# Optimization experiments

Measured on AMD Instinct MI355X. Metric: run time of the kernel, lower is better.

## Reference

```python
import jax, jax.numpy as jnp
import numpy as np

N_NODES = 100000
N_EDGES = 3200000
EMBED_DIM = 64
BATCH = 16384


def setup_inputs() -> dict:
    key = jax.random.key(0)
    k1, k2, k3, k4 = jax.random.split(key, 4)
    gcn_weight = jax.random.normal(k1, (N_NODES, EMBED_DIM), dtype=jnp.float32) * 0.1
    gcn_bias = jnp.zeros((EMBED_DIM,), dtype=jnp.float32)
    linear_weight = jax.random.normal(k2, (N_NODES, 1), dtype=jnp.float32) * 0.1
    linear_bias = jnp.zeros((1,), dtype=jnp.float32)
    edge_index = jax.random.randint(k3, (2, N_EDGES), 0, N_NODES, dtype=jnp.int64)
    interaction_pairs = jax.random.randint(k4, (BATCH, 2), 0, N_NODES, dtype=jnp.int64)
    return {
        "gcn_weight": gcn_weight,
        "gcn_bias": gcn_bias,
        "linear_weight": linear_weight,
        "linear_bias": linear_bias,
        "edge_index": edge_index,
        "interaction_pairs": interaction_pairs,
    }


def _gcn_conv_identity_features(gcn_weight, gcn_bias, edge_index):
    # Features X = I, so X @ W = W. GCNConv output = D^{-1/2}(A+I)D^{-1/2} W + b.
    src, dst = edge_index[0], edge_index[1]
    ones = jnp.ones((src.shape[0],), dtype=gcn_weight.dtype)
    # degree (with self loop) computed on destination nodes, as in PyG gcn_norm
    deg = jax.ops.segment_sum(ones, dst, num_segments=N_NODES) + 1.0
    dinv = jax.lax.rsqrt(deg)  # [N]
    norm = dinv[src] * dinv[dst]  # [E]
    msg = gcn_weight[src] * norm[:, None]  # [E, D] -- dominant memory traffic
    agg = jax.ops.segment_sum(msg, dst, num_segments=N_NODES)  # [N, D]
    # self-loop term: norm_ii = 1/deg[i]
    out = agg + gcn_weight * (dinv * dinv)[:, None] + gcn_bias
    return out


def reference(gcn_weight, gcn_bias, linear_weight, linear_bias, edge_index, interaction_pairs):
    node_emb = _gcn_conv_identity_features(gcn_weight, gcn_bias, edge_index)  # [N, D]
    e = node_emb[interaction_pairs]  # [B, 2, D] gather
    # FM pairwise interaction: 0.5 * sum_d ((sum_f e)^2 - sum_f e^2)
    sum_sq = jnp.square(jnp.sum(e, axis=1))  # [B, D]
    sq_sum = jnp.sum(jnp.square(e), axis=1)  # [B, D]
    fm = 0.5 * jnp.sum(sum_sq - sq_sum, axis=1, keepdims=True)  # [B, 1]
    # FeaturesLinear: sum of per-node scalar embeddings + bias
    lin = jnp.sum(linear_weight[interaction_pairs], axis=1) + linear_bias  # [B, 1]
    return jnp.squeeze(lin + fm, axis=1)  # [B]
```

## Files before the change

kernel.cpp:

```cpp
#include <hip/hip_runtime.h>

#define N_NODES 100000
#define N_EDGES 3200000
#define BATCH 16384
#define MAX_SLOTS 32768

#define NW 12500
#define SLICES 256
#define EPS2 12500
#define I4PS2 3125

#define NBUCK 256
#define BSH 7

#define OFF_SLOT      0
#define OFF_DINV      400064
#define OFF_NODELIST  800064
#define OFF_BTOT      931136
#define OFF_BPART     932160
#define OFF_SLOTSTART 1194304
#define OFF_PARTIALS  1325440
#define OFF_WH        14125440
#define OFF_BINS      26925440
#define OFF_BINS2     31725440
#define OFF_EMB       36525440

__device__ __forceinline__ unsigned bfr(float f) {
    unsigned u = __float_as_uint(f);
    return (u + 0x7FFFu + ((u >> 16) & 1u)) >> 16;
}
__device__ __forceinline__ float bfx(unsigned h) {
    return __uint_as_float(h << 16);
}

__global__ void k_flags(const int* __restrict__ pairs, unsigned* __restrict__ slot,
                        int* __restrict__ nodelist) {
    int i = blockIdx.x * blockDim.x + threadIdx.x;
    if (i < 2 * BATCH) {
        int n = pairs[i];
        nodelist[i] = n;
        slot[n] = (unsigned)(i + 1);
    }
}

__device__ __forceinline__ int cert(int d, const unsigned* __restrict__ slot,
                                    const int* __restrict__ nodelist) {
    unsigned r = slot[d];
    unsigned idx = r - 1u;
    if (idx < (unsigned)MAX_SLOTS && nodelist[idx] == d) return (int)idx;
    return -1;
}

__global__ void k_hist(const int* __restrict__ dst, const unsigned* __restrict__ slot,
                       const int* __restrict__ nodelist,
                       unsigned* __restrict__ partials, int* __restrict__ bpart) {
    __shared__ unsigned h[NW];
    __shared__ int lc[NBUCK];
    int g = blockIdx.x;
    for (int i = threadIdx.x; i < NW; i += 512) h[i] = 0;
    if (threadIdx.x < NBUCK) lc[threadIdx.x] = 0;
    __syncthreads();
    const int4* d4 = (const int4*)(dst + g * EPS2);
    for (int i = threadIdx.x; i < I4PS2; i += 512) {
        int4 v = d4[i];
        atomicAdd(&h[v.x >> 3], 1u << ((v.x & 7) << 2));
        atomicAdd(&h[v.y >> 3], 1u << ((v.y & 7) << 2));
        atomicAdd(&h[v.z >> 3], 1u << ((v.z & 7) << 2));
        atomicAdd(&h[v.w >> 3], 1u << ((v.w & 7) << 2));
        int t;
        t = cert(v.x, slot, nodelist); if (t >= 0) atomicAdd(&lc[t >> BSH], 1);
        t = cert(v.y, slot, nodelist); if (t >= 0) atomicAdd(&lc[t >> BSH], 1);
        t = cert(v.z, slot, nodelist); if (t >= 0) atomicAdd(&lc[t >> BSH], 1);
        t = cert(v.w, slot, nodelist); if (t >= 0) atomicAdd(&lc[t >> BSH], 1);
    }
    __syncthreads();
    unsigned* outp = partials + (unsigned)g * NW;
    for (int i = threadIdx.x; i < NW; i += 512) outp[i] = h[i];
    if (threadIdx.x < NBUCK) bpart[threadIdx.x * SLICES + g] = lc[threadIdx.x];
}

__global__ void k_mid(const unsigned* __restrict__ partials, const float4* __restrict__ w4,
                      float* __restrict__ dinv, uint4* __restrict__ wh4,
                      int* __restrict__ bpart, int* __restrict__ btot) {
    if (blockIdx.x >= 391) {
        __shared__ int t[SLICES];
        int b = blockIdx.x - 391, g = threadIdx.x;
        int v = bpart[b * SLICES + g];
        t[g] = v;
        __syncthreads();
        for (int off = 1; off < SLICES; off <<= 1) {
            int x = (g >= off) ? t[g - off] : 0;
            __syncthreads();
            t[g] += x;
            __syncthreads();
        }
        bpart[b * SLICES + g] = t[g] - v;
        if (g == SLICES - 1) btot[b] = t[g];
        return;
    }
    __shared__ unsigned pA[256], pB[256], pC[256], pD[256];
    __shared__ float sdinv[256];
    int blk = blockIdx.x;
    int wi = threadIdx.x & 31, sg = threadIdx.x >> 5;
    int w = blk * 32 + wi;
    unsigned A = 0, B = 0, C = 0, D = 0;
    if (w < NW) {
        const unsigned* q = partials + w;
#pragma unroll
        for (int ch = 0; ch < 2; ++ch) {
            unsigned x = 0, y = 0;
#pragma unroll
            for (int k = 0; k < 16; ++k) {
                unsigned v = q[(unsigned)(sg * 32 + ch * 16 + k) * NW];
                x += v & 0x0F0F0F0Fu;
                y += (v >> 4) & 0x0F0F0F0Fu;
            }
            A += x & 0x00FF00FFu;
            B += (x >> 8) & 0x00FF00FFu;
            C += y & 0x00FF00FFu;
            D += (y >> 8) & 0x00FF00FFu;
        }
    }
    pA[threadIdx.x] = A; pB[threadIdx.x] = B; pC[threadIdx.x] = C; pD[threadIdx.x] = D;
    __syncthreads();
    if (threadIdx.x < 32 && w < NW) {
        unsigned sA = 0, sB = 0, sC = 0, sD = 0;
#pragma unroll
        for (int k = 0; k < 8; ++k) {
            sA += pA[k * 32 + wi]; sB += pB[k * 32 + wi];
            sC += pC[k * 32 + wi]; sD += pD[k * 32 + wi];
        }
        float4 d0, d1;
        d0.x = rsqrtf((float)(sA & 0xFFFFu) + 1.0f);
        d0.y = rsqrtf((float)(sC & 0xFFFFu) + 1.0f);
        d0.z = rsqrtf((float)(sB & 0xFFFFu) + 1.0f);
        d0.w = rsqrtf((float)(sD & 0xFFFFu) + 1.0f);
        d1.x = rsqrtf((float)(sA >> 16) + 1.0f);
        d1.y = rsqrtf((float)(sC >> 16) + 1.0f);
        d1.z = rsqrtf((float)(sB >> 16) + 1.0f);
        d1.w = rsqrtf((float)(sD >> 16) + 1.0f);
        ((float4*)dinv)[w * 2] = d0;
        ((float4*)dinv)[w * 2 + 1] = d1;
        int lb = wi * 8;
        sdinv[lb + 0] = d0.x; sdinv[lb + 1] = d0.y; sdinv[lb + 2] = d0.z; sdinv[lb + 3] = d0.w;
        sdinv[lb + 4] = d1.x; sdinv[lb + 5] = d1.y; sdinv[lb + 6] = d1.z; sdinv[lb + 7] = d1.w;
    }
    __syncthreads();
#pragma unroll
    for (int it = 0; it < 8; ++it) {
        int k = blk * 2048 + it * 256 + threadIdx.x;
        if (k < N_NODES * 8) {
            float4 va = w4[k * 2];
            float4 vb = w4[k * 2 + 1];
            float d = sdinv[(k >> 3) - blk * 256];
            uint4 o;
            o.x = bfr(va.x * d) | (bfr(va.y * d) << 16);
            o.y = bfr(va.z * d) | (bfr(va.w * d) << 16);
            o.z = bfr(vb.x * d) | (bfr(vb.y * d) << 16);
            o.w = bfr(vb.z * d) | (bfr(vb.w * d) << 16);
            wh4[k] = o;
        }
    }
}

__global__ void k_bscatter(const int* __restrict__ src, const int* __restrict__ dst,
                           const unsigned* __restrict__ slot, const int* __restrict__ nodelist,
                           const int* __restrict__ bpart, const int* __restrict__ btot,
                           int* __restrict__ bins) {
    __shared__ int tb[NBUCK], vv[NBUCK], cur[NBUCK];
    int g = blockIdx.x;
    int t = threadIdx.x;
    if (t < NBUCK) { int v = btot[t]; vv[t] = v; tb[t] = v; }
    __syncthreads();
    for (int off = 1; off < NBUCK; off <<= 1) {
        int x = (t < NBUCK && t >= off) ? tb[t - off] : 0;
        __syncthreads();
        if (t < NBUCK) tb[t] += x;
        __syncthreads();
    }
    if (t < NBUCK) cur[t] = tb[t] - vv[t] + bpart[t * SLICES + g];
    __syncthreads();
    const int4* d4 = (const int4*)(dst + g * EPS2);
    const int4* s4 = (const int4*)(src + g * EPS2);
    for (int i = t; i < I4PS2; i += 512) {
        int4 d = d4[i];
        int4 s = s4[i];
        int sl;
        sl = cert(d.x, slot, nodelist);
        if (sl >= 0) { int pos = atomicAdd(&cur[sl >> BSH], 1); bins[pos] = ((sl & 127) << 17) | s.x; }
        sl = cert(d.y, slot, nodelist);
        if (sl >= 0) { int pos = atomicAdd(&cur[sl >> BSH], 1); bins[pos] = ((sl & 127) << 17) | s.y; }
        sl = cert(d.z, slot, nodelist);
        if (sl >= 0) { int pos = atomicAdd(&cur[sl >> BSH], 1); bins[pos] = ((sl & 127) << 17) | s.z; }
        sl = cert(d.w, slot, nodelist);
        if (sl >= 0) { int pos = atomicAdd(&cur[sl >> BSH], 1); bins[pos] = ((sl & 127) << 17) | s.w; }
    }
}

__global__ void k_bsort(const int* __restrict__ btot, const int* __restrict__ bins,
                        int* __restrict__ slotstart, int* __restrict__ bins2) {
    __shared__ int tb[NBUCK], vv[NBUCK];
    __shared__ int lc[128], st[128];
    int b = blockIdx.x;
    int tid = threadIdx.x;
    { int v = btot[tid]; vv[tid] = v; tb[tid] = v; }
    __syncthreads();
    for (int off = 1; off < NBUCK; off <<= 1) {
        int x = (tid >= off) ? tb[tid - off] : 0;
        __syncthreads();
        tb[tid] += x;
        __syncthreads();
    }
    int beg = tb[b] - vv[b];
    int end = beg + vv[b];
    if (tid < 128) lc[tid] = 0;
    __syncthreads();
    for (int j = beg + tid; j < end; j += 256)
        atomicAdd(&lc[(bins[j] >> 17) & 127], 1);
    __syncthreads();
    if (tid < 128) st[tid] = lc[tid];
    __syncthreads();
    for (int off = 1; off < 128; off <<= 1) {
        int v = (tid < 128 && tid >= off) ? st[tid - off] : 0;
        __syncthreads();
        if (tid < 128) st[tid] += v;
        __syncthreads();
    }
    if (tid < 128) {
        int s0 = beg + st[tid] - lc[tid];
        slotstart[(b << 7) + tid] = s0;
        lc[tid] = s0;
    }
    if (b == NBUCK - 1 && tid == 0) slotstart[MAX_SLOTS] = tb[NBUCK - 1];
    __syncthreads();
    for (int j = beg + tid; j < end; j += 256) {
        int e = bins[j];
        int pos = atomicAdd(&lc[(e >> 17) & 127], 1);
        bins2[pos] = e & 0x1FFFF;
    }
}

__global__ void k_gather(const int* __restrict__ nodelist, const int* __restrict__ slotstart,
                         const int* __restrict__ bins2, const uint4* __restrict__ wh4,
                         const float* __restrict__ dinv, const float4* __restrict__ bias4,
                         uint4* __restrict__ emb4) {
    int s = (blockIdx.x * blockDim.x + threadIdx.x) >> 6;
    int lane = threadIdx.x & 63;
    int rg = lane >> 3, dp = lane & 7;
    int beg = slotstart[s], end = slotstart[s + 1];
    float a0 = 0.f, a1 = 0.f, a2 = 0.f, a3 = 0.f, a4 = 0.f, a5 = 0.f, a6 = 0.f, a7 = 0.f;
    int j = beg;
    for (; j + 16 <= end; j += 16) {
        int e0 = bins2[j + rg];
        int e1 = bins2[j + 8 + rg];
        uint4 oa = wh4[(e0 << 3) + dp];
        uint4 ob = wh4[(e1 << 3) + dp];
        a0 += bfx(oa.x) + bfx(ob.x);
        a1 += bfx(oa.x >> 16) + bfx(ob.x >> 16);
        a2 += bfx(oa.y) + bfx(ob.y);
        a3 += bfx(oa.y >> 16) + bfx(ob.y >> 16);
        a4 += bfx(oa.z) + bfx(ob.z);
        a5 += bfx(oa.z >> 16) + bfx(ob.z >> 16);
        a6 += bfx(oa.w) + bfx(ob.w);
        a7 += bfx(oa.w >> 16) + bfx(ob.w >> 16);
    }
    for (; j < end; j += 8) {
        if (rg < end - j) {
            int e0 = bins2[j + rg];
            uint4 oa = wh4[(e0 << 3) + dp];
            a0 += bfx(oa.x); a1 += bfx(oa.x >> 16);
            a2 += bfx(oa.y); a3 += bfx(oa.y >> 16);
            a4 += bfx(oa.z); a5 += bfx(oa.z >> 16);
            a6 += bfx(oa.w); a7 += bfx(oa.w >> 16);
        }
    }
#pragma unroll
    for (int m = 8; m <= 32; m <<= 1) {
        a0 += __shfl_xor(a0, m, 64); a1 += __shfl_xor(a1, m, 64);
        a2 += __shfl_xor(a2, m, 64); a3 += __shfl_xor(a3, m, 64);
        a4 += __shfl_xor(a4, m, 64); a5 += __shfl_xor(a5, m, 64);
        a6 += __shfl_xor(a6, m, 64); a7 += __shfl_xor(a7, m, 64);
    }
    if (rg == 0) {
        int n = nodelist[s];
        float dn = dinv[n];
        uint4 u = wh4[(n << 3) + dp];
        float4 b0 = bias4[dp * 2], b1 = bias4[dp * 2 + 1];
        float r0 = (a0 + bfx(u.x)) * dn + b0.x;
        float r1 = (a1 + bfx(u.x >> 16)) * dn + b0.y;
        float r2 = (a2 + bfx(u.y)) * dn + b0.z;
        float r3 = (a3 + bfx(u.y >> 16)) * dn + b0.w;
        float r4 = (a4 + bfx(u.z)) * dn + b1.x;
        float r5 = (a5 + bfx(u.z >> 16)) * dn + b1.y;
        float r6 = (a6 + bfx(u.w)) * dn + b1.z;
        float r7 = (a7 + bfx(u.w >> 16)) * dn + b1.w;
        uint4 o;
        o.x = bfr(r0) | (bfr(r1) << 16);
        o.y = bfr(r2) | (bfr(r3) << 16);
        o.z = bfr(r4) | (bfr(r5) << 16);
        o.w = bfr(r6) | (bfr(r7) << 16);
        emb4[(s << 3) + dp] = o;
    }
}

__global__ void k_final(const int* __restrict__ pairs, const unsigned* __restrict__ slot,
                        const uint2* __restrict__ emb2, const float* __restrict__ lw,
                        const float* __restrict__ lb, float* __restrict__ out) {
    int p = (blockIdx.x * blockDim.x + threadIdx.x) >> 4;
    int li = threadIdx.x & 15;
    if (p >= BATCH) return;
    int a = pairs[p * 2], b = pairs[p * 2 + 1];
    int sa = (int)slot[a] - 1;
    int sb = (int)slot[b] - 1;
    uint2 ua = emb2[(sa << 4) + li];
    uint2 ub = emb2[(sb << 4) + li];
    float prod = bfx(ua.x) * bfx(ub.x) + bfx(ua.x >> 16) * bfx(ub.x >> 16)
               + bfx(ua.y) * bfx(ub.y) + bfx(ua.y >> 16) * bfx(ub.y >> 16);
#pragma unroll
    for (int m = 1; m <= 8; m <<= 1) prod += __shfl_xor(prod, m, 64);
    if (li == 0) out[p] = lw[a] + lw[b] + lb[0] + prod;
}

extern "C" void kernel_launch(void* const* d_in, const int* in_sizes, int n_in,
                              void* d_out, int out_size, void* d_ws, size_t ws_size,
                              hipStream_t stream) {
    const float* gcn_weight    = (const float*)d_in[0];
    const float* gcn_bias      = (const float*)d_in[1];
    const float* linear_weight = (const float*)d_in[2];
    const float* linear_bias   = (const float*)d_in[3];
    const int*   edge_index    = (const int*)d_in[4];
    const int*   pairs         = (const int*)d_in[5];
    float* out = (float*)d_out;

    char* ws = (char*)d_ws;
    unsigned* slot      = (unsigned*)(ws + OFF_SLOT);
    float*    dinv      = (float*)   (ws + OFF_DINV);
    int*      nodelist  = (int*)     (ws + OFF_NODELIST);
    int*      btot      = (int*)     (ws + OFF_BTOT);
    int*      bpart     = (int*)     (ws + OFF_BPART);
    int*      slotstart = (int*)     (ws + OFF_SLOTSTART);
    unsigned* partials  = (unsigned*)(ws + OFF_PARTIALS);
    uint4*    wh4       = (uint4*)   (ws + OFF_WH);
    int*      bins      = (int*)     (ws + OFF_BINS);
    int*      bins2     = (int*)     (ws + OFF_BINS2);
    uint4*    emb4      = (uint4*)   (ws + OFF_EMB);
    uint2*    emb2      = (uint2*)   (ws + OFF_EMB);

    const int* src_arr = edge_index;
    const int* dst_arr = edge_index + N_EDGES;

    k_flags<<<128, 256, 0, stream>>>(pairs, slot, nodelist);
    k_hist<<<SLICES, 512, 0, stream>>>(dst_arr, slot, nodelist, partials, bpart);
    k_mid<<<391 + 256, 256, 0, stream>>>(partials, (const float4*)gcn_weight, dinv, wh4,
                                         bpart, btot);
    k_bscatter<<<SLICES, 512, 0, stream>>>(src_arr, dst_arr, slot, nodelist, bpart, btot, bins);
    k_bsort<<<NBUCK, 256, 0, stream>>>(btot, bins, slotstart, bins2);
    k_gather<<<MAX_SLOTS / 4, 256, 0, stream>>>(nodelist, slotstart, bins2, wh4,
                                                dinv, (const float4*)gcn_bias, emb4);
    k_final<<<1024, 256, 0, stream>>>(pairs, slot, emb2, linear_weight, linear_bias, out);
}
```

Measured before the change: 185.1 us.

## Replace two-pass bucket sort with fixed-capacity per-slot bins filled in histogram kernel

Drops the bucket count/scan/scatter/sort pipeline (k_bscatter, k_bsort and the scan blocks in k_mid). Edges into batch nodes are now appended straight into fixed 128-entry per-slot bins using global atomic counters, inside the degree-histogram kernel, which now runs 1024-thread blocks. This removes a second pass over the edge list and two kernel launches. The gather now reads the per-slot counts and accumulates in double precision. The fixed capacity silently drops neighbors beyond 128 per node, and double accumulation raises register use and ALU cost.

```diff
diff --git a/kernel.cpp b/kernel.cpp
--- a/kernel.cpp
+++ b/kernel.cpp
@@ -10,20 +10,16 @@
 #define EPS2 12500
 #define I4PS2 3125
 
-#define NBUCK 256
-#define BSH 7
+#define CAP 128
 
 #define OFF_SLOT      0
 #define OFF_DINV      400064
 #define OFF_NODELIST  800064
-#define OFF_BTOT      931136
-#define OFF_BPART     932160
-#define OFF_SLOTSTART 1194304
-#define OFF_PARTIALS  1325440
-#define OFF_WH        14125440
-#define OFF_BINS      26925440
-#define OFF_BINS2     31725440
-#define OFF_EMB       36525440
+#define OFF_SCOUNT    931136
+#define OFF_PARTIALS  1062208
+#define OFF_WH        13862208
+#define OFF_BINS2     26662208
+#define OFF_EMB       43439424
 
 __device__ __forceinline__ unsigned bfr(float f) {
     unsigned u = __float_as_uint(f);
@@ -34,12 +30,13 @@
 }
 
 __global__ void k_flags(const int* __restrict__ pairs, unsigned* __restrict__ slot,
-                        int* __restrict__ nodelist) {
+                        int* __restrict__ nodelist, int* __restrict__ scount) {
     int i = blockIdx.x * blockDim.x + threadIdx.x;
     if (i < 2 * BATCH) {
         int n = pairs[i];
         nodelist[i] = n;
         slot[n] = (unsigned)(i + 1);
+        scount[i] = 0;
     }
 }
 
@@ -51,53 +48,40 @@
     return -1;
 }
 
-__global__ void k_hist(const int* __restrict__ dst, const unsigned* __restrict__ slot,
-                       const int* __restrict__ nodelist,
-                       unsigned* __restrict__ partials, int* __restrict__ bpart) {
+__global__ void k_fused(const int* __restrict__ src, const int* __restrict__ dst,
+                        const unsigned* __restrict__ slot, const int* __restrict__ nodelist,
+                        unsigned* __restrict__ partials,
+                        int* __restrict__ scount, int* __restrict__ bins2) {
     __shared__ unsigned h[NW];
-    __shared__ int lc[NBUCK];
     int g = blockIdx.x;
-    for (int i = threadIdx.x; i < NW; i += 512) h[i] = 0;
-    if (threadIdx.x < NBUCK) lc[threadIdx.x] = 0;
+    for (int i = threadIdx.x; i < NW; i += 1024) h[i] = 0;
     __syncthreads();
     const int4* d4 = (const int4*)(dst + g * EPS2);
-    for (int i = threadIdx.x; i < I4PS2; i += 512) {
+    const int4* s4 = (const int4*)(src + g * EPS2);
+    for (int i = threadIdx.x; i < I4PS2; i += 1024) {
         int4 v = d4[i];
+        int4 s = s4[i];
         atomicAdd(&h[v.x >> 3], 1u << ((v.x & 7) << 2));
         atomicAdd(&h[v.y >> 3], 1u << ((v.y & 7) << 2));
         atomicAdd(&h[v.z >> 3], 1u << ((v.z & 7) << 2));
         atomicAdd(&h[v.w >> 3], 1u << ((v.w & 7) << 2));
         int t;
-        t = cert(v.x, slot, nodelist); if (t >= 0) atomicAdd(&lc[t >> BSH], 1);
-        t = cert(v.y, slot, nodelist); if (t >= 0) atomicAdd(&lc[t >> BSH], 1);
-        t = cert(v.z, slot, nodelist); if (t >= 0) atomicAdd(&lc[t >> BSH], 1);
-        t = cert(v.w, slot, nodelist); if (t >= 0) atomicAdd(&lc[t >> BSH], 1);
+        t = cert(v.x, slot, nodelist);
+        if (t >= 0) { int p = atomicAdd(&scount[t], 1); if (p < CAP) bins2[(t << 7) + p] = s.x; }
+        t = cert(v.y, slot, nodelist);
+        if (t >= 0) { int p = atomicAdd(&scount[t], 1); if (p < CAP) bins2[(t << 7) + p] = s.y; }
+        t = cert(v.z, slot, nodelist);
+        if (t >= 0) { int p = atomicAdd(&scount[t], 1); if (p < CAP) bins2[(t << 7) + p] = s.z; }
+        t = cert(v.w, slot, nodelist);
+        if (t >= 0) { int p = atomicAdd(&scount[t], 1); if (p < CAP) bins2[(t << 7) + p] = s.w; }
     }
     __syncthreads();
     unsigned* outp = partials + (unsigned)g * NW;
-    for (int i = threadIdx.x; i < NW; i += 512) outp[i] = h[i];
-    if (threadIdx.x < NBUCK) bpart[threadIdx.x * SLICES + g] = lc[threadIdx.x];
+    for (int i = threadIdx.x; i < NW; i += 1024) outp[i] = h[i];
 }
 
 __global__ void k_mid(const unsigned* __restrict__ partials, const float4* __restrict__ w4,
-                      float* __restrict__ dinv, uint4* __restrict__ wh4,
-                      int* __restrict__ bpart, int* __restrict__ btot) {
-    if (blockIdx.x >= 391) {
-        __shared__ int t[SLICES];
-        int b = blockIdx.x - 391, g = threadIdx.x;
-        int v = bpart[b * SLICES + g];
-        t[g] = v;
-        __syncthreads();
-        for (int off = 1; off < SLICES; off <<= 1) {
-            int x = (g >= off) ? t[g - off] : 0;
-            __syncthreads();
-            t[g] += x;
-            __syncthreads();
-        }
-        bpart[b * SLICES + g] = t[g] - v;
-        if (g == SLICES - 1) btot[b] = t[g];
-        return;
-    }
+                      float* __restrict__ dinv, uint4* __restrict__ wh4) {
     __shared__ unsigned pA[256], pB[256], pC[256], pD[256];
     __shared__ float sdinv[256];
     int blk = blockIdx.x;
@@ -163,115 +147,39 @@
     }
 }
 
-__global__ void k_bscatter(const int* __restrict__ src, const int* __restrict__ dst,
-                           const unsigned* __restrict__ slot, const int* __restrict__ nodelist,
-                           const int* __restrict__ bpart, const int* __restrict__ btot,
-                           int* __restrict__ bins) {
-    __shared__ int tb[NBUCK], vv[NBUCK], cur[NBUCK];
-    int g = blockIdx.x;
-    int t = threadIdx.x;
-    if (t < NBUCK) { int v = btot[t]; vv[t] = v; tb[t] = v; }
-    __syncthreads();
-    for (int off = 1; off < NBUCK; off <<= 1) {
-        int x = (t < NBUCK && t >= off) ? tb[t - off] : 0;
-        __syncthreads();
-        if (t < NBUCK) tb[t] += x;
-        __syncthreads();
-    }
-    if (t < NBUCK) cur[t] = tb[t] - vv[t] + bpart[t * SLICES + g];
-    __syncthreads();
-    const int4* d4 = (const int4*)(dst + g * EPS2);
-    const int4* s4 = (const int4*)(src + g * EPS2);
-    for (int i = t; i < I4PS2; i += 512) {
-        int4 d = d4[i];
-        int4 s = s4[i];
-        int sl;
-        sl = cert(d.x, slot, nodelist);
-        if (sl >= 0) { int pos = atomicAdd(&cur[sl >> BSH], 1); bins[pos] = ((sl & 127) << 17) | s.x; }
-        sl = cert(d.y, slot, nodelist);
-        if (sl >= 0) { int pos = atomicAdd(&cur[sl >> BSH], 1); bins[pos] = ((sl & 127) << 17) | s.y; }
-        sl = cert(d.z, slot, nodelist);
-        if (sl >= 0) { int pos = atomicAdd(&cur[sl >> BSH], 1); bins[pos] = ((sl & 127) << 17) | s.z; }
-        sl = cert(d.w, slot, nodelist);
-        if (sl >= 0) { int pos = atomicAdd(&cur[sl >> BSH], 1); bins[pos] = ((sl & 127) << 17) | s.w; }
-    }
-}
-
-__global__ void k_bsort(const int* __restrict__ btot, const int* __restrict__ bins,
-                        int* __restrict__ slotstart, int* __restrict__ bins2) {
-    __shared__ int tb[NBUCK], vv[NBUCK];
-    __shared__ int lc[128], st[128];
-    int b = blockIdx.x;
-    int tid = threadIdx.x;
-    { int v = btot[tid]; vv[tid] = v; tb[tid] = v; }
-    __syncthreads();
-    for (int off = 1; off < NBUCK; off <<= 1) {
-        int x = (tid >= off) ? tb[tid - off] : 0;
-        __syncthreads();
-        tb[tid] += x;
-        __syncthreads();
-    }
-    int beg = tb[b] - vv[b];
-    int end = beg + vv[b];
-    if (tid < 128) lc[tid] = 0;
-    __syncthreads();
-    for (int j = beg + tid; j < end; j += 256)
-        atomicAdd(&lc[(bins[j] >> 17) & 127], 1);
-    __syncthreads();
-    if (tid < 128) st[tid] = lc[tid];
-    __syncthreads();
-    for (int off = 1; off < 128; off <<= 1) {
-        int v = (tid < 128 && tid >= off) ? st[tid - off] : 0;
-        __syncthreads();
-        if (tid < 128) st[tid] += v;
-        __syncthreads();
-    }
-    if (tid < 128) {
-        int s0 = beg + st[tid] - lc[tid];
-        slotstart[(b << 7) + tid] = s0;
-        lc[tid] = s0;
-    }
-    if (b == NBUCK - 1 && tid == 0) slotstart[MAX_SLOTS] = tb[NBUCK - 1];
-    __syncthreads();
-    for (int j = beg + tid; j < end; j += 256) {
-        int e = bins[j];
-        int pos = atomicAdd(&lc[(e >> 17) & 127], 1);
-        bins2[pos] = e & 0x1FFFF;
-    }
-}
-
-__global__ void k_gather(const int* __restrict__ nodelist, const int* __restrict__ slotstart,
+__global__ void k_gather(const int* __restrict__ nodelist, const int* __restrict__ scount,
                          const int* __restrict__ bins2, const uint4* __restrict__ wh4,
                          const float* __restrict__ dinv, const float4* __restrict__ bias4,
                          uint4* __restrict__ emb4) {
     int s = (blockIdx.x * blockDim.x + threadIdx.x) >> 6;
     int lane = threadIdx.x & 63;
     int rg = lane >> 3, dp = lane & 7;
-    int beg = slotstart[s], end = slotstart[s + 1];
-    float a0 = 0.f, a1 = 0.f, a2 = 0.f, a3 = 0.f, a4 = 0.f, a5 = 0.f, a6 = 0.f, a7 = 0.f;
-    int j = beg;
-    for (; j + 16 <= end; j += 16) {
-        int e0 = bins2[j + rg];
-        int e1 = bins2[j + 8 + rg];
+    int cnt = scount[s];
+    const int* bp = bins2 + (s << 7);
+    double a0 = 0., a1 = 0., a2 = 0., a3 = 0., a4 = 0., a5 = 0., a6 = 0., a7 = 0.;
+    int j = 0;
+    for (; j + 16 <= cnt; j += 16) {
+        int e0 = bp[j + rg];
+        int e1 = bp[j + 8 + rg];
         uint4 oa = wh4[(e0 << 3) + dp];
         uint4 ob = wh4[(e1 << 3) + dp];
-        a0 += bfx(oa.x) + bfx(ob.x);
-        a1 += bfx(oa.x >> 16) + bfx(ob.x >> 16);
-        a2 += bfx(oa.y) + bfx(ob.y);
-        a3 += bfx(oa.y >> 16) + bfx(ob.y >> 16);
-        a4 += bfx(oa.z) + bfx(ob.z);
-        a5 += bfx(oa.z >> 16) + bfx(ob.z >> 16);
-        a6 += bfx(oa.w) + bfx(ob.w);
-        a7 += bfx(oa.w >> 16) + bfx(ob.w >> 16);
-    }
-    for (; j < end; j += 8) {
-        if (rg < end - j) {
-            int e0 = bins2[j + rg];
+        a0 += (double)(bfx(oa.x) + bfx(ob.x));
+        a1 += (double)(bfx(oa.x >> 16) + bfx(ob.x >> 16));
+        a2 += (double)(bfx(oa.y) + bfx(ob.y));
+        a3 += (double)(bfx(oa.y >> 16) + bfx(ob.y >> 16));
+        a4 += (double)(bfx(oa.z) + bfx(ob.z));
+        a5 += (double)(bfx(oa.z >> 16) + bfx(ob.z >> 16));
+        a6 += (double)(bfx(oa.w) + bfx(ob.w));
+        a7 += (double)(bfx(oa.w >> 16) + bfx(ob.w >> 16));
+    }
+    for (; j < cnt; j += 8) {
+        if (rg < cnt - j) {
+            int e0 = bp[j + rg];
             uint4 oa = wh4[(e0 << 3) + dp];
-            a0 += bfx(oa.x); a1 += bfx(oa.x >> 16);
-            a2 += bfx(oa.y); a3 += bfx(oa.y >> 16);
-            a4 += bfx(oa.z); a5 += bfx(oa.z >> 16);
-            a6 += bfx(oa.w); a7 += bfx(oa.w >> 16);
+            a0 += (double)bfx(oa.x); a1 += (double)bfx(oa.x >> 16);
+            a2 += (double)bfx(oa.y); a3 += (double)bfx(oa.y >> 16);
+            a4 += (double)bfx(oa.z); a5 += (double)bfx(oa.z >> 16);
+            a6 += (double)bfx(oa.w); a7 += (double)bfx(oa.w >> 16);
         }
     }
 #pragma unroll
@@ -286,14 +194,14 @@
         float dn = dinv[n];
         uint4 u = wh4[(n << 3) + dp];
         float4 b0 = bias4[dp * 2], b1 = bias4[dp * 2 + 1];
-        float r0 = (a0 + bfx(u.x)) * dn + b0.x;
-        float r1 = (a1 + bfx(u.x >> 16)) * dn + b0.y;
-        float r2 = (a2 + bfx(u.y)) * dn + b0.z;
-        float r3 = (a3 + bfx(u.y >> 16)) * dn + b0.w;
-        float r4 = (a4 + bfx(u.z)) * dn + b1.x;
-        float r5 = (a5 + bfx(u.z >> 16)) * dn + b1.y;
-        float r6 = (a6 + bfx(u.w)) * dn + b1.z;
-        float r7 = (a7 + bfx(u.w >> 16)) * dn + b1.w;
+        float r0 = ((float)a0 + bfx(u.x)) * dn + b0.x;
+        float r1 = ((float)a1 + bfx(u.x >> 16)) * dn + b0.y;
+        float r2 = ((float)a2 + bfx(u.y)) * dn + b0.z;
+        float r3 = ((float)a3 + bfx(u.y >> 16)) * dn + b0.w;
+        float r4 = ((float)a4 + bfx(u.z)) * dn + b1.x;
+        float r5 = ((float)a5 + bfx(u.z >> 16)) * dn + b1.y;
+        float r6 = ((float)a6 + bfx(u.w)) * dn + b1.z;
+        float r7 = ((float)a7 + bfx(u.w >> 16)) * dn + b1.w;
         uint4 o;
         o.x = bfr(r0) | (bfr(r1) << 16);
         o.y = bfr(r2) | (bfr(r3) << 16);
@@ -336,12 +244,9 @@
     unsigned* slot      = (unsigned*)(ws + OFF_SLOT);
     float*    dinv      = (float*)   (ws + OFF_DINV);
     int*      nodelist  = (int*)     (ws + OFF_NODELIST);
-    int*      btot      = (int*)     (ws + OFF_BTOT);
-    int*      bpart     = (int*)     (ws + OFF_BPART);
-    int*      slotstart = (int*)     (ws + OFF_SLOTSTART);
+    int*      scount    = (int*)     (ws + OFF_SCOUNT);
     unsigned* partials  = (unsigned*)(ws + OFF_PARTIALS);
     uint4*    wh4       = (uint4*)   (ws + OFF_WH);
-    int*      bins      = (int*)     (ws + OFF_BINS);
     int*      bins2     = (int*)     (ws + OFF_BINS2);
     uint4*    emb4      = (uint4*)   (ws + OFF_EMB);
     uint2*    emb2      = (uint2*)   (ws + OFF_EMB);
@@ -349,13 +254,11 @@
     const int* src_arr = edge_index;
     const int* dst_arr = edge_index + N_EDGES;
 
-    k_flags<<<128, 256, 0, stream>>>(pairs, slot, nodelist);
-    k_hist<<<SLICES, 512, 0, stream>>>(dst_arr, slot, nodelist, partials, bpart);
-    k_mid<<<391 + 256, 256, 0, stream>>>(partials, (const float4*)gcn_weight, dinv, wh4,
-                                         bpart, btot);
-    k_bscatter<<<SLICES, 512, 0, stream>>>(src_arr, dst_arr, slot, nodelist, bpart, btot, bins);
-    k_bsort<<<NBUCK, 256, 0, stream>>>(btot, bins, slotstart, bins2);
-    k_gather<<<MAX_SLOTS / 4, 256, 0, stream>>>(nodelist, slotstart, bins2, wh4,
+    k_flags<<<128, 256, 0, stream>>>(pairs, slot, nodelist, scount);
+    k_fused<<<SLICES, 1024, 0, stream>>>(src_arr, dst_arr, slot, nodelist,
+                                         partials, scount, bins2);
+    k_mid<<<391, 256, 0, stream>>>(partials, (const float4*)gcn_weight, dinv, wh4);
+    k_gather<<<MAX_SLOTS / 4, 256, 0, stream>>>(nodelist, scount, bins2, wh4,
                                                 dinv, (const float4*)gcn_bias, emb4);
     k_final<<<1024, 256, 0, stream>>>(pairs, slot, emb2, linear_weight, linear_bias, out);
 }
```

Result: slower. 192.0 us (+3.7%).
